# Kernel optimization log

Measured on AMD Instinct MI355X. Metric: run time of the kernel, lower is better.

## Reference

```python
import jax, jax.numpy as jnp
import numpy as np

EMBED_DIM = 768
NUM_HEADS = 12
HEAD_DIM = EMBED_DIM // NUM_HEADS


def setup_inputs() -> dict:
    key = jax.random.key(0)
    ks = jax.random.split(key, 9)
    B, S, E = 8, 1024, EMBED_DIM
    scale = 1.0 / np.sqrt(E)
    inputs = jax.random.normal(ks[0], (B, S, E), dtype=jnp.float32)
    Wq = jax.random.normal(ks[1], (E, E), dtype=jnp.float32) * scale
    Wk = jax.random.normal(ks[2], (E, E), dtype=jnp.float32) * scale
    Wv = jax.random.normal(ks[3], (E, E), dtype=jnp.float32) * scale
    Wo = jax.random.normal(ks[4], (E, E), dtype=jnp.float32) * scale
    bq = jnp.zeros((E,), dtype=jnp.float32)
    bk = jnp.zeros((E,), dtype=jnp.float32)
    bv = jnp.zeros((E,), dtype=jnp.float32)
    bo = jnp.zeros((E,), dtype=jnp.float32)
    return {"inputs": inputs, "Wq": Wq, "bq": bq, "Wk": Wk, "bk": bk,
            "Wv": Wv, "bv": bv, "Wo": Wo, "bo": bo}


def reference(inputs, Wq, bq, Wk, bk, Wv, bv, Wo, bo):
    B, S, E = inputs.shape
    H, D = NUM_HEADS, HEAD_DIM

    def split_heads(x):  # [B,S,E] -> [B,H,S,D]
        return x.reshape(B, S, H, D).transpose(0, 2, 1, 3)

    q = split_heads(inputs @ Wq + bq)
    k = split_heads(inputs @ Wk + bk)
    v = split_heads(inputs @ Wv + bv)

    # scaled dot-product attention; note: scale uses sqrt(last dim of key) = sqrt(D)
    score = jnp.einsum('bhqd,bhkd->bhqk', q, k) / jnp.sqrt(jnp.float32(D))
    weights = jax.nn.softmax(score, axis=-1)
    attn = jnp.einsum('bhqk,bhkd->bhqd', weights, v)  # [B,H,S,D]

    concat = attn.transpose(0, 2, 1, 3).reshape(B, S, E)
    return concat @ Wo + bo
```

## Files before the change

### kernel.cpp

```cpp
#include <hip/hip_runtime.h>
#include <hip/hip_bf16.h>
#include <cstddef>

#define E_DIM  768
#define S_LEN  1024
#define NHEADS 12
#define HDIM   64
#define BATCH  8
#define TOKENS (BATCH * S_LEN)
#define WELEMS (E_DIM * E_DIM)

typedef short bf16x8 __attribute__((ext_vector_type(8)));
typedef short bf16x4 __attribute__((ext_vector_type(4)));
typedef float f32x4  __attribute__((ext_vector_type(4)));

#define MFMA16(a, b, c) __builtin_amdgcn_mfma_f32_16x16x32_bf16((a), (b), (c), 0, 0, 0)

#define GLD_LDS16(gp, lp)                                                  \
    __builtin_amdgcn_global_load_lds(                                      \
        (const __attribute__((address_space(1))) void*)(gp),               \
        (__attribute__((address_space(3))) void*)(lp), 16, 0, 0)

static __device__ __forceinline__ short f2bf(float f) {
    union { float f; unsigned int u; } cv; cv.f = f;
    unsigned int u = cv.u + 0x7fffu + ((cv.u >> 16) & 1u);
    return (short)(u >> 16);
}

__global__ __launch_bounds__(256) void transpose_w(
    const float* __restrict__ s0, const float* __restrict__ s1,
    const float* __restrict__ s2, short* __restrict__ dst)
{
    const float* S = (blockIdx.z == 0) ? s0 : (blockIdx.z == 1) ? s1 : s2;
    short* D = dst + (size_t)blockIdx.z * WELEMS;
    __shared__ float t[64][65];
    const int r = threadIdx.x >> 2, c0 = (threadIdx.x & 3) * 16;
    const int br = blockIdx.x * 64, bc = blockIdx.y * 64;
    #pragma unroll
    for (int j = 0; j < 4; ++j) {
        float4 v = *(const float4*)&S[(size_t)(br + r) * E_DIM + bc + c0 + j * 4];
        t[r][c0 + j * 4 + 0] = v.x; t[r][c0 + j * 4 + 1] = v.y;
        t[r][c0 + j * 4 + 2] = v.z; t[r][c0 + j * 4 + 3] = v.w;
    }
    __syncthreads();
    #pragma unroll
    for (int half = 0; half < 2; ++half) {
        bf16x8 o;
        #pragma unroll
        for (int j = 0; j < 8; ++j) o[j] = f2bf(t[c0 + half * 8 + j][r]);
        *(bf16x8*)&D[(size_t)(bc + r) * E_DIM + br + c0 + half * 8] = o;
    }
}

__global__ __launch_bounds__(256) void gemm_qkv_kernel(
    const float* __restrict__ X, const short* __restrict__ Wt,
    const float* __restrict__ bq, const float* __restrict__ bk,
    const float* __restrict__ bv, short* __restrict__ oq,
    short* __restrict__ ok, short* __restrict__ ov)
{
    __shared__ __align__(16) short As[128 * 64];
    __shared__ __align__(16) short Bs[128 * 64];

    const int tid  = threadIdx.x;
    const int wave = tid >> 6, lane = tid & 63;
    const int quad = lane >> 4, l16 = lane & 15;
    const int bm = blockIdx.x * 128;
    const int by = blockIdx.y;
    const int wsel = by / 6;
    const int nb = (by % 6) * 128;
    const short* wt = Wt + (size_t)wsel * WELEMS;
    const float* bias = (wsel == 0) ? bq : (wsel == 1) ? bk : bv;
    short* outp = (wsel == 0) ? oq : (wsel == 1) ? ok : ov;

    const int wm = (wave >> 1) * 64, wn = (wave & 1) * 64;

    f32x4 acc[4][4];
    #pragma unroll
    for (int mt = 0; mt < 4; ++mt)
        #pragma unroll
        for (int nt = 0; nt < 4; ++nt) acc[mt][nt] = (f32x4){0.f, 0.f, 0.f, 0.f};

    for (int k0 = 0; k0 < E_DIM; k0 += 64) {
        float4 ax[4][2];
        #pragma unroll
        for (int i = 0; i < 4; ++i) {
            const int slot = i * 256 + tid;
            const int row = slot >> 3, cl = slot & 7;
            const float4* gp = (const float4*)&X[(size_t)(bm + row) * E_DIM + k0 + cl * 8];
            ax[i][0] = gp[0]; ax[i][1] = gp[1];
        }
        __syncthreads();
        #pragma unroll
        for (int i = 0; i < 4; ++i) {
            const int slot = i * 256 + tid;
            const int row = slot >> 3, cl = slot & 7, cg = cl ^ (row & 7);
            GLD_LDS16(&wt[(size_t)(nb + row) * E_DIM + k0 + cg * 8], &Bs[slot * 8]);
        }
        #pragma unroll
        for (int i = 0; i < 4; ++i) {
            const int slot = i * 256 + tid;
            const int row = slot >> 3, cl = slot & 7, cs = cl ^ (row & 7);
            bf16x8 v8;
            v8[0] = f2bf(ax[i][0].x); v8[1] = f2bf(ax[i][0].y);
            v8[2] = f2bf(ax[i][0].z); v8[3] = f2bf(ax[i][0].w);
            v8[4] = f2bf(ax[i][1].x); v8[5] = f2bf(ax[i][1].y);
            v8[6] = f2bf(ax[i][1].z); v8[7] = f2bf(ax[i][1].w);
            *(bf16x8*)&As[row * 64 + cs * 8] = v8;
        }
        __syncthreads();

        #pragma unroll
        for (int ks = 0; ks < 2; ++ks) {
            bf16x8 a[4], b[4];
            #pragma unroll
            for (int mt = 0; mt < 4; ++mt) {
                const int row = wm + mt * 16 + l16;
                const int c = (ks * 4 + quad) ^ (row & 7);
                a[mt] = *(const bf16x8*)&As[row * 64 + c * 8];
            }
            #pragma unroll
            for (int nt = 0; nt < 4; ++nt) {
                const int row = wn + nt * 16 + l16;
                const int c = (ks * 4 + quad) ^ (row & 7);
                b[nt] = *(const bf16x8*)&Bs[row * 64 + c * 8];
            }
            #pragma unroll
            for (int mt = 0; mt < 4; ++mt)
                #pragma unroll
                for (int nt = 0; nt < 4; ++nt)
                    acc[mt][nt] = MFMA16(a[mt], b[nt], acc[mt][nt]);
        }
    }

    const float qscale = (wsel == 0) ? 0.125f : 1.0f;
    #pragma unroll
    for (int nt = 0; nt < 4; ++nt) {
        const int ncol = nb + wn + nt * 16 + l16;
        const float bvv = bias[ncol];
        const int h = ncol >> 6, d = ncol & (HDIM - 1);
        #pragma unroll
        for (int mt = 0; mt < 4; ++mt) {
            const int grow = bm + wm + mt * 16 + quad * 4;
            if (wsel < 2) {
                #pragma unroll
                for (int r = 0; r < 4; ++r) {
                    const int g = grow + r, b = g >> 10, s = g & (S_LEN - 1);
                    outp[((size_t)(b * NHEADS + h) * S_LEN + s) * HDIM + d] =
                        f2bf((acc[mt][nt][r] + bvv) * qscale);
                }
            } else {
                const int b = grow >> 10, s0 = grow & (S_LEN - 1);
                bf16x4 pv;
                #pragma unroll
                for (int r = 0; r < 4; ++r) pv[r] = f2bf(acc[mt][nt][r] + bvv);
                *(bf16x4*)&outp[((size_t)(b * NHEADS + h) * HDIM + d) * S_LEN + s0] = pv;
            }
        }
    }
}

__global__ __launch_bounds__(256) void gemm_out_kernel(
    const short* __restrict__ A, const short* __restrict__ Wt,
    const float* __restrict__ bias, float* __restrict__ out)
{
    __shared__ __align__(16) short As[128 * 64];
    __shared__ __align__(16) short Bs[128 * 64];

    const int tid  = threadIdx.x;
    const int wave = tid >> 6, lane = tid & 63;
    const int quad = lane >> 4, l16 = lane & 15;
    const int bm = blockIdx.x * 128, nb = blockIdx.y * 128;
    const int wm = (wave >> 1) * 64, wn = (wave & 1) * 64;

    f32x4 acc[4][4];
    #pragma unroll
    for (int mt = 0; mt < 4; ++mt)
        #pragma unroll
        for (int nt = 0; nt < 4; ++nt) acc[mt][nt] = (f32x4){0.f, 0.f, 0.f, 0.f};

    for (int k0 = 0; k0 < E_DIM; k0 += 64) {
        __syncthreads();
        #pragma unroll
        for (int i = 0; i < 4; ++i) {
            const int slot = i * 256 + tid;
            const int row = slot >> 3, cl = slot & 7, cg = cl ^ (row & 7);
            GLD_LDS16(&A[(size_t)(bm + row) * E_DIM + k0 + cg * 8], &As[slot * 8]);
        }
        #pragma unroll
        for (int i = 0; i < 4; ++i) {
            const int slot = i * 256 + tid;
            const int row = slot >> 3, cl = slot & 7, cg = cl ^ (row & 7);
            GLD_LDS16(&Wt[(size_t)(nb + row) * E_DIM + k0 + cg * 8], &Bs[slot * 8]);
        }
        __syncthreads();

        #pragma unroll
        for (int ks = 0; ks < 2; ++ks) {
            bf16x8 a[4], b[4];
            #pragma unroll
            for (int mt = 0; mt < 4; ++mt) {
                const int row = wm + mt * 16 + l16;
                const int c = (ks * 4 + quad) ^ (row & 7);
                a[mt] = *(const bf16x8*)&As[row * 64 + c * 8];
            }
            #pragma unroll
            for (int nt = 0; nt < 4; ++nt) {
                const int row = wn + nt * 16 + l16;
                const int c = (ks * 4 + quad) ^ (row & 7);
                b[nt] = *(const bf16x8*)&Bs[row * 64 + c * 8];
            }
            #pragma unroll
            for (int mt = 0; mt < 4; ++mt)
                #pragma unroll
                for (int nt = 0; nt < 4; ++nt)
                    acc[mt][nt] = MFMA16(a[mt], b[nt], acc[mt][nt]);
        }
    }

    #pragma unroll
    for (int nt = 0; nt < 4; ++nt) {
        const int ncol = nb + wn + nt * 16 + l16;
        const float bvv = bias[ncol];
        #pragma unroll
        for (int mt = 0; mt < 4; ++mt) {
            const int grow = bm + wm + mt * 16 + quad * 4;
            #pragma unroll
            for (int r = 0; r < 4; ++r)
                out[(size_t)(grow + r) * E_DIM + ncol] = acc[mt][nt][r] + bvv;
        }
    }
}

__global__ __launch_bounds__(256) void attn_kernel(
    const short* __restrict__ Q, const short* __restrict__ K,
    const short* __restrict__ V, short* __restrict__ O)
{
    __shared__ __align__(16) short Qs[64 * 72];
    __shared__ __align__(16) short Ps[64 * 72];
    __shared__ __align__(16) short Ks[64 * 64];
    __shared__ __align__(16) short Vt[64 * 64];

    const int tid  = threadIdx.x;
    const int wave = tid >> 6, lane = tid & 63;
    const int quad = lane >> 4, l16 = lane & 15;
    const int q0 = blockIdx.x * 64;
    const int bh = blockIdx.y;
    const size_t base = (size_t)bh * S_LEN * HDIM;
    const short* Qb = Q + base;
    const short* Kb = K + base;
    const short* Vb = V + base;

    {
        const int r = tid >> 2, c = (tid & 3) * 16;
        bf16x8 a0 = *(const bf16x8*)&Qb[(size_t)(q0 + r) * HDIM + c];
        bf16x8 a1 = *(const bf16x8*)&Qb[(size_t)(q0 + r) * HDIM + c + 8];
        *(bf16x8*)&Qs[r * 72 + c]     = a0;
        *(bf16x8*)&Qs[r * 72 + c + 8] = a1;
    }
    __syncthreads();
    const bf16x8 qa0 = *(const bf16x8*)&Qs[(wave * 16 + l16) * 72 + quad * 8];
    const bf16x8 qa1 = *(const bf16x8*)&Qs[(wave * 16 + l16) * 72 + quad * 8 + 32];

    bf16x8 ones;
    #pragma unroll
    for (int j = 0; j < 8; ++j) ones[j] = (short)0x3F80;

    f32x4 oacc[4], lacc;
    #pragma unroll
    for (int nt = 0; nt < 4; ++nt) oacc[nt] = (f32x4){0.f, 0.f, 0.f, 0.f};
    lacc = (f32x4){0.f, 0.f, 0.f, 0.f};

    for (int kt = 0; kt < S_LEN; kt += 64) {
        __syncthreads();
        #pragma unroll
        for (int i = 0; i < 2; ++i) {
            const int slot = i * 256 + tid;
            const int row = slot >> 3, cl = slot & 7, cg = cl ^ (row & 7);
            GLD_LDS16(&Kb[(size_t)(kt + row) * HDIM + cg * 8], &Ks[slot * 8]);
        }
        #pragma unroll
        for (int i = 0; i < 2; ++i) {
            const int slot = i * 256 + tid;
            const int row = slot >> 3, cl = slot & 7, cg = cl ^ (row & 7);
            GLD_LDS16(&Vb[(size_t)row * S_LEN + kt + cg * 8], &Vt[slot * 8]);
        }
        __syncthreads();

        f32x4 sc[4];
        #pragma unroll
        for (int nt = 0; nt < 4; ++nt) sc[nt] = (f32x4){0.f, 0.f, 0.f, 0.f};
        #pragma unroll
        for (int ks = 0; ks < 2; ++ks) {
            const bf16x8 qa = ks ? qa1 : qa0;
            #pragma unroll
            for (int nt = 0; nt < 4; ++nt) {
                const int row = nt * 16 + l16;
                const int c = (ks * 4 + quad) ^ (row & 7);
                const bf16x8 kf = *(const bf16x8*)&Ks[row * 64 + c * 8];
                sc[nt] = MFMA16(qa, kf, sc[nt]);
            }
        }

        const int prow = wave * 16 + quad * 4;
        #pragma unroll
        for (int nt = 0; nt < 4; ++nt)
            #pragma unroll
            for (int r = 0; r < 4; ++r)
                Ps[(prow + r) * 72 + nt * 16 + l16] = f2bf(__expf(sc[nt][r]));

        const bf16x8 pa0 = *(const bf16x8*)&Ps[(wave * 16 + l16) * 72 + quad * 8];
        const bf16x8 pa1 = *(const bf16x8*)&Ps[(wave * 16 + l16) * 72 + quad * 8 + 32];

        #pragma unroll
        for (int ks = 0; ks < 2; ++ks) {
            const bf16x8 pa = ks ? pa1 : pa0;
            #pragma unroll
            for (int nt = 0; nt < 4; ++nt) {
                const int row = nt * 16 + l16;
                const int c = (ks * 4 + quad) ^ (row & 7);
                const bf16x8 vf = *(const bf16x8*)&Vt[row * 64 + c * 8];
                oacc[nt] = MFMA16(pa, vf, oacc[nt]);
            }
            lacc = MFMA16(pa, ones, lacc);
        }
    }

    const int b = bh / NHEADS, h = bh - b * NHEADS;
    #pragma unroll
    for (int nt = 0; nt < 4; ++nt) {
        #pragma unroll
        for (int r = 0; r < 4; ++r) {
            const int qrow = q0 + wave * 16 + quad * 4 + r;
            const float val = oacc[nt][r] / lacc[r];
            O[(size_t)(b * S_LEN + qrow) * E_DIM + h * HDIM + nt * 16 + l16] = f2bf(val);
        }
    }
}

extern "C" void kernel_launch(void* const* d_in, const int* in_sizes, int n_in,
                              void* d_out, int out_size, void* d_ws, size_t ws_size,
                              hipStream_t stream) {
    const float* X  = (const float*)d_in[0];
    const float* Wq = (const float*)d_in[1];
    const float* bq = (const float*)d_in[2];
    const float* Wk = (const float*)d_in[3];
    const float* bk = (const float*)d_in[4];
    const float* Wv = (const float*)d_in[5];
    const float* bv = (const float*)d_in[6];
    const float* Wo = (const float*)d_in[7];
    const float* bo = (const float*)d_in[8];
    float* out = (float*)d_out;

    const size_t t = (size_t)TOKENS * E_DIM;
    short* q    = (short*)d_ws;
    short* k    = q + t;
    short* vT   = k + t;
    short* attn = vT + t;
    short* wt_qkv = attn;
    short* wt_o = q;

    transpose_w<<<dim3(12, 12, 3), 256, 0, stream>>>(Wq, Wk, Wv, wt_qkv);
    gemm_qkv_kernel<<<dim3(TOKENS / 128, 18), 256, 0, stream>>>(
        X, wt_qkv, bq, bk, bv, q, k, vT);
    attn_kernel<<<dim3(S_LEN / 64, BATCH * NHEADS), 256, 0, stream>>>(q, k, vT, attn);
    transpose_w<<<dim3(12, 12, 1), 256, 0, stream>>>(Wo, Wo, Wo, wt_o);
    gemm_out_kernel<<<dim3(TOKENS / 128, 6), 256, 0, stream>>>(attn, wt_o, bo, out);
}
```

Baseline: 230.0 us.

## Pre-convert X to bf16, merge weight transposes, double attention query tile

```diff
diff --git a/kernel.cpp b/kernel.cpp
--- a/kernel.cpp
+++ b/kernel.cpp
@@ -27,12 +27,26 @@
     return (short)(u >> 16);
 }
 
+__global__ __launch_bounds__(256) void xcvt_kernel(
+    const float* __restrict__ X, short* __restrict__ Y)
+{
+    const size_t i = ((size_t)blockIdx.x * 256 + threadIdx.x) * 8;
+    const float4 a = *(const float4*)&X[i];
+    const float4 b = *(const float4*)&X[i + 4];
+    bf16x8 o;
+    o[0] = f2bf(a.x); o[1] = f2bf(a.y); o[2] = f2bf(a.z); o[3] = f2bf(a.w);
+    o[4] = f2bf(b.x); o[5] = f2bf(b.y); o[6] = f2bf(b.z); o[7] = f2bf(b.w);
+    *(bf16x8*)&Y[i] = o;
+}
+
 __global__ __launch_bounds__(256) void transpose_w(
     const float* __restrict__ s0, const float* __restrict__ s1,
-    const float* __restrict__ s2, short* __restrict__ dst)
+    const float* __restrict__ s2, const float* __restrict__ s3,
+    short* __restrict__ dst)
 {
-    const float* S = (blockIdx.z == 0) ? s0 : (blockIdx.z == 1) ? s1 : s2;
-    short* D = dst + (size_t)blockIdx.z * WELEMS;
+    const int z = blockIdx.z;
+    const float* S = (z == 0) ? s0 : (z == 1) ? s1 : (z == 2) ? s2 : s3;
+    short* D = dst + (size_t)z * WELEMS;
     __shared__ float t[64][65];
     const int r = threadIdx.x >> 2, c0 = (threadIdx.x & 3) * 16;
     const int br = blockIdx.x * 64, bc = blockIdx.y * 64;
@@ -52,8 +66,9 @@
     }
 }
 
-__global__ __launch_bounds__(256) void gemm_qkv_kernel(
-    const float* __restrict__ X, const short* __restrict__ Wt,
+template<bool AF32>
+__global__ __launch_bounds__(256) void gemm_qkv_t(
+    const void* __restrict__ Ap, const short* __restrict__ Wt,
     const float* __restrict__ bq, const float* __restrict__ bk,
     const float* __restrict__ bv, short* __restrict__ oq,
     short* __restrict__ ok, short* __restrict__ ov)
@@ -71,7 +86,6 @@
     const short* wt = Wt + (size_t)wsel * WELEMS;
     const float* bias = (wsel == 0) ? bq : (wsel == 1) ? bk : bv;
     short* outp = (wsel == 0) ? oq : (wsel == 1) ? ok : ov;
-
     const int wm = (wave >> 1) * 64, wn = (wave & 1) * 64;
 
     f32x4 acc[4][4];
@@ -81,31 +95,49 @@
         for (int nt = 0; nt < 4; ++nt) acc[mt][nt] = (f32x4){0.f, 0.f, 0.f, 0.f};
 
     for (int k0 = 0; k0 < E_DIM; k0 += 64) {
-        float4 ax[4][2];
-        #pragma unroll
-        for (int i = 0; i < 4; ++i) {
-            const int slot = i * 256 + tid;
-            const int row = slot >> 3, cl = slot & 7;
-            const float4* gp = (const float4*)&X[(size_t)(bm + row) * E_DIM + k0 + cl * 8];
-            ax[i][0] = gp[0]; ax[i][1] = gp[1];
-        }
-        __syncthreads();
-        #pragma unroll
-        for (int i = 0; i < 4; ++i) {
-            const int slot = i * 256 + tid;
-            const int row = slot >> 3, cl = slot & 7, cg = cl ^ (row & 7);
-            GLD_LDS16(&wt[(size_t)(nb + row) * E_DIM + k0 + cg * 8], &Bs[slot * 8]);
-        }
-        #pragma unroll
-        for (int i = 0; i < 4; ++i) {
-            const int slot = i * 256 + tid;
-            const int row = slot >> 3, cl = slot & 7, cs = cl ^ (row & 7);
-            bf16x8 v8;
-            v8[0] = f2bf(ax[i][0].x); v8[1] = f2bf(ax[i][0].y);
-            v8[2] = f2bf(ax[i][0].z); v8[3] = f2bf(ax[i][0].w);
-            v8[4] = f2bf(ax[i][1].x); v8[5] = f2bf(ax[i][1].y);
-            v8[6] = f2bf(ax[i][1].z); v8[7] = f2bf(ax[i][1].w);
-            *(bf16x8*)&As[row * 64 + cs * 8] = v8;
+        if (AF32) {
+            const float* A = (const float*)Ap;
+            float4 ax[4][2];
+            #pragma unroll
+            for (int i = 0; i < 4; ++i) {
+                const int slot = i * 256 + tid;
+                const int row = slot >> 3, cl = slot & 7;
+                const float4* gp = (const float4*)&A[(size_t)(bm + row) * E_DIM + k0 + cl * 8];
+                ax[i][0] = gp[0]; ax[i][1] = gp[1];
+            }
+            __syncthreads();
+            #pragma unroll
+            for (int i = 0; i < 4; ++i) {
+                const int slot = i * 256 + tid;
+                const int row = slot >> 3, cl = slot & 7, cg = cl ^ (row & 7);
+                GLD_LDS16(&wt[(size_t)(nb + row) * E_DIM + k0 + cg * 8], &Bs[slot * 8]);
+            }
+            #pragma unroll
+            for (int i = 0; i < 4; ++i) {
+                const int slot = i * 256 + tid;
+                const int row = slot >> 3, cl = slot & 7, cs = cl ^ (row & 7);
+                bf16x8 v8;
+                v8[0] = f2bf(ax[i][0].x); v8[1] = f2bf(ax[i][0].y);
+                v8[2] = f2bf(ax[i][0].z); v8[3] = f2bf(ax[i][0].w);
+                v8[4] = f2bf(ax[i][1].x); v8[5] = f2bf(ax[i][1].y);
+                v8[6] = f2bf(ax[i][1].z); v8[7] = f2bf(ax[i][1].w);
+                *(bf16x8*)&As[row * 64 + cs * 8] = v8;
+            }
+        } else {
+            const short* A = (const short*)Ap;
+            __syncthreads();
+            #pragma unroll
+            for (int i = 0; i < 4; ++i) {
+                const int slot = i * 256 + tid;
+                const int row = slot >> 3, cl = slot & 7, cg = cl ^ (row & 7);
+                GLD_LDS16(&A[(size_t)(bm + row) * E_DIM + k0 + cg * 8], &As[slot * 8]);
+            }
+            #pragma unroll
+            for (int i = 0; i < 4; ++i) {
+                const int slot = i * 256 + tid;
+                const int row = slot >> 3, cl = slot & 7, cg = cl ^ (row & 7);
+                GLD_LDS16(&wt[(size_t)(nb + row) * E_DIM + k0 + cg * 8], &Bs[slot * 8]);
+            }
         }
         __syncthreads();
 
@@ -235,40 +267,47 @@
     const short* __restrict__ Q, const short* __restrict__ K,
     const short* __restrict__ V, short* __restrict__ O)
 {
-    __shared__ __align__(16) short Qs[64 * 72];
-    __shared__ __align__(16) short Ps[64 * 72];
+    __shared__ __align__(16) short Qs[128 * 72];
+    __shared__ __align__(16) short Ps[128 * 72];
     __shared__ __align__(16) short Ks[64 * 64];
     __shared__ __align__(16) short Vt[64 * 64];
 
     const int tid  = threadIdx.x;
     const int wave = tid >> 6, lane = tid & 63;
     const int quad = lane >> 4, l16 = lane & 15;
-    const int q0 = blockIdx.x * 64;
+    const int q0 = blockIdx.x * 128;
     const int bh = blockIdx.y;
     const size_t base = (size_t)bh * S_LEN * HDIM;
     const short* Qb = Q + base;
     const short* Kb = K + base;
     const short* Vb = V + base;
 
-    {
-        const int r = tid >> 2, c = (tid & 3) * 16;
-        bf16x8 a0 = *(const bf16x8*)&Qb[(size_t)(q0 + r) * HDIM + c];
-        bf16x8 a1 = *(const bf16x8*)&Qb[(size_t)(q0 + r) * HDIM + c + 8];
-        *(bf16x8*)&Qs[r * 72 + c]     = a0;
-        *(bf16x8*)&Qs[r * 72 + c + 8] = a1;
+    #pragma unroll
+    for (int i = 0; i < 4; ++i) {
+        const int slot = i * 256 + tid;
+        const int row = slot >> 3, cl = slot & 7;
+        bf16x8 v = *(const bf16x8*)&Qb[(size_t)(q0 + row) * HDIM + cl * 8];
+        *(bf16x8*)&Qs[row * 72 + cl * 8] = v;
     }
     __syncthreads();
-    const bf16x8 qa0 = *(const bf16x8*)&Qs[(wave * 16 + l16) * 72 + quad * 8];
-    const bf16x8 qa1 = *(const bf16x8*)&Qs[(wave * 16 + l16) * 72 + quad * 8 + 32];
+    bf16x8 qa[2][2];
+    #pragma unroll
+    for (int mt = 0; mt < 2; ++mt)
+        #pragma unroll
+        for (int ks = 0; ks < 2; ++ks)
+            qa[mt][ks] = *(const bf16x8*)&Qs[(wave * 32 + mt * 16 + l16) * 72 + ks * 32 + quad * 8];
 
     bf16x8 ones;
     #pragma unroll
     for (int j = 0; j < 8; ++j) ones[j] = (short)0x3F80;
 
-    f32x4 oacc[4], lacc;
-    #pragma unroll
-    for (int nt = 0; nt < 4; ++nt) oacc[nt] = (f32x4){0.f, 0.f, 0.f, 0.f};
-    lacc = (f32x4){0.f, 0.f, 0.f, 0.f};
+    f32x4 oacc[2][4], lacc[2];
+    #pragma unroll
+    for (int mt = 0; mt < 2; ++mt) {
+        #pragma unroll
+        for (int nt = 0; nt < 4; ++nt) oacc[mt][nt] = (f32x4){0.f, 0.f, 0.f, 0.f};
+        lacc[mt] = (f32x4){0.f, 0.f, 0.f, 0.f};
+    }
 
     for (int kt = 0; kt < S_LEN; kt += 64) {
         __syncthreads();
@@ -286,55 +325,68 @@
         }
         __syncthreads();
 
-        f32x4 sc[4];
-        #pragma unroll
-        for (int nt = 0; nt < 4; ++nt) sc[nt] = (f32x4){0.f, 0.f, 0.f, 0.f};
-        #pragma unroll
-        for (int ks = 0; ks < 2; ++ks) {
-            const bf16x8 qa = ks ? qa1 : qa0;
+        f32x4 sc[2][4];
+        #pragma unroll
+        for (int mt = 0; mt < 2; ++mt)
+            #pragma unroll
+            for (int nt = 0; nt < 4; ++nt) sc[mt][nt] = (f32x4){0.f, 0.f, 0.f, 0.f};
+        #pragma unroll
+        for (int ks = 0; ks < 2; ++ks)
             #pragma unroll
             for (int nt = 0; nt < 4; ++nt) {
                 const int row = nt * 16 + l16;
                 const int c = (ks * 4 + quad) ^ (row & 7);
                 const bf16x8 kf = *(const bf16x8*)&Ks[row * 64 + c * 8];
-                sc[nt] = MFMA16(qa, kf, sc[nt]);
-            }
-        }
-
-        const int prow = wave * 16 + quad * 4;
-        #pragma unroll
-        for (int nt = 0; nt < 4; ++nt)
-            #pragma unroll
-            for (int r = 0; r < 4; ++r)
-                Ps[(prow + r) * 72 + nt * 16 + l16] = f2bf(__expf(sc[nt][r]));
-
-        const bf16x8 pa0 = *(const bf16x8*)&Ps[(wave * 16 + l16) * 72 + quad * 8];
-        const bf16x8 pa1 = *(const bf16x8*)&Ps[(wave * 16 + l16) * 72 + quad * 8 + 32];
+                #pragma unroll
+                for (int mt = 0; mt < 2; ++mt)
+                    sc[mt][nt] = MFMA16(qa[mt][ks], kf, sc[mt][nt]);
+            }
+
+        #pragma unroll
+        for (int mt = 0; mt < 2; ++mt) {
+            const int prow = wave * 32 + mt * 16 + quad * 4;
+            #pragma unroll
+            for (int nt = 0; nt < 4; ++nt)
+                #pragma unroll
+                for (int r = 0; r < 4; ++r)
+                    Ps[(prow + r) * 72 + nt * 16 + l16] = f2bf(__expf(sc[mt][nt][r]));
+        }
+
+        bf16x8 pa[2][2];
+        #pragma unroll
+        for (int mt = 0; mt < 2; ++mt)
+            #pragma unroll
+            for (int ks = 0; ks < 2; ++ks)
+                pa[mt][ks] = *(const bf16x8*)&Ps[(wave * 32 + mt * 16 + l16) * 72 + ks * 32 + quad * 8];
 
         #pragma unroll
         for (int ks = 0; ks < 2; ++ks) {
-            const bf16x8 pa = ks ? pa1 : pa0;
             #pragma unroll
             for (int nt = 0; nt < 4; ++nt) {
                 const int row = nt * 16 + l16;
                 const int c = (ks * 4 + quad) ^ (row & 7);
                 const bf16x8 vf = *(const bf16x8*)&Vt[row * 64 + c * 8];
-                oacc[nt] = MFMA16(pa, vf, oacc[nt]);
-            }
-            lacc = MFMA16(pa, ones, lacc);
+                #pragma unroll
+                for (int mt = 0; mt < 2; ++mt)
+                    oacc[mt][nt] = MFMA16(pa[mt][ks], vf, oacc[mt][nt]);
+            }
+            #pragma unroll
+            for (int mt = 0; mt < 2; ++mt)
+                lacc[mt] = MFMA16(pa[mt][ks], ones, lacc[mt]);
         }
     }
 
     const int b = bh / NHEADS, h = bh - b * NHEADS;
     #pragma unroll
-    for (int nt = 0; nt < 4; ++nt) {
-        #pragma unroll
-        for (int r = 0; r < 4; ++r) {
-            const int qrow = q0 + wave * 16 + quad * 4 + r;
-            const float val = oacc[nt][r] / lacc[r];
-            O[(size_t)(b * S_LEN + qrow) * E_DIM + h * HDIM + nt * 16 + l16] = f2bf(val);
-        }
-    }
+    for (int mt = 0; mt < 2; ++mt)
+        #pragma unroll
+        for (int nt = 0; nt < 4; ++nt)
+            #pragma unroll
+            for (int r = 0; r < 4; ++r) {
+                const int qrow = q0 + wave * 32 + mt * 16 + quad * 4 + r;
+                const float val = oacc[mt][nt][r] / lacc[mt][r];
+                O[(size_t)(b * S_LEN + qrow) * E_DIM + h * HDIM + nt * 16 + l16] = f2bf(val);
+            }
 }
 
 extern "C" void kernel_launch(void* const* d_in, const int* in_sizes, int n_in,
@@ -356,13 +408,26 @@
     short* k    = q + t;
     short* vT   = k + t;
     short* attn = vT + t;
-    short* wt_qkv = attn;
-    short* wt_o = q;
-
-    transpose_w<<<dim3(12, 12, 3), 256, 0, stream>>>(Wq, Wk, Wv, wt_qkv);
-    gemm_qkv_kernel<<<dim3(TOKENS / 128, 18), 256, 0, stream>>>(
-        X, wt_qkv, bq, bk, bv, q, k, vT);
-    attn_kernel<<<dim3(S_LEN / 64, BATCH * NHEADS), 256, 0, stream>>>(q, k, vT, attn);
-    transpose_w<<<dim3(12, 12, 1), 256, 0, stream>>>(Wo, Wo, Wo, wt_o);
-    gemm_out_kernel<<<dim3(TOKENS / 128, 6), 256, 0, stream>>>(attn, wt_o, bo, out);
-}
+
+    const size_t fast_need = (5 * t + 4 * (size_t)WELEMS) * 2;
+    if (ws_size >= fast_need) {
+        short* wt4 = attn + t;
+        short* xbf = wt4 + 4 * (size_t)WELEMS;
+        xcvt_kernel<<<(TOKENS * E_DIM / 8) / 256, 256, 0, stream>>>(X, xbf);
+        transpose_w<<<dim3(12, 12, 4), 256, 0, stream>>>(Wq, Wk, Wv, Wo, wt4);
+        gemm_qkv_t<false><<<dim3(TOKENS / 128, 18), 256, 0, stream>>>(
+            xbf, wt4, bq, bk, bv, q, k, vT);
+        attn_kernel<<<dim3(S_LEN / 128, BATCH * NHEADS), 256, 0, stream>>>(q, k, vT, attn);
+        gemm_out_kernel<<<dim3(TOKENS / 128, 6), 256, 0, stream>>>(
+            attn, wt4 + 3 * (size_t)WELEMS, bo, out);
+    } else {
+        short* wt_qkv = attn;
+        short* wt_o   = q;
+        transpose_w<<<dim3(12, 12, 3), 256, 0, stream>>>(Wq, Wk, Wv, Wv, wt_qkv);
+        gemm_qkv_t<true><<<dim3(TOKENS / 128, 18), 256, 0, stream>>>(
+            X, wt_qkv, bq, bk, bv, q, k, vT);
+        attn_kernel<<<dim3(S_LEN / 128, BATCH * NHEADS), 256, 0, stream>>>(q, k, vT, attn);
+        transpose_w<<<dim3(12, 12, 1), 256, 0, stream>>>(Wo, Wo, Wo, Wo, wt_o);
+        gemm_out_kernel<<<dim3(TOKENS / 128, 6), 256, 0, stream>>>(attn, wt_o, bo, out);
+    }
+}
```

Result: faster. 210.8 us (-8.3%).
